# Optimization experiments

Hardware: AMD Instinct MI355X
Metric: run time of the kernel (lower is better)

The kernel has to match this reference:

```python
import jax, jax.numpy as jnp
import numpy as np

EPS = 1e-12
PERP_EPS = 1e-10


def setup_inputs() -> dict:
    key = jax.random.key(0)
    k1, k2, k3 = jax.random.split(key, 3)
    B, D, H, W = 32, 64, 32, 32
    K = 1024
    inputs = jax.random.normal(k1, (B, D, H, W), dtype=jnp.float32)
    codebooks = jax.random.normal(k2, (K, D), dtype=jnp.float32)
    noise = jax.random.normal(k3, (B * H * W, D), dtype=jnp.float32)
    return {"inputs": inputs, "codebooks": codebooks, "noise": noise}


def reference(inputs, codebooks, noise):
    B, D, H, W = inputs.shape
    K = codebooks.shape[0]
    # NCHW -> NHWC -> (N, D)
    x = jnp.transpose(inputs, (0, 2, 3, 1)).reshape(-1, D)
    distances = (
        jnp.sum(x * x, axis=1, keepdims=True)
        - 2.0 * jnp.einsum("nd,kd->nk", x, codebooks)
        + jnp.sum(codebooks * codebooks, axis=1)[None, :]
    )
    min_indices = jnp.argmin(distances, axis=1)  # (N,)
    best_entries = codebooks[min_indices]  # gather, (N, D)
    # per-row norm-matched noise injection (NSVQ)
    norm_best = jnp.sqrt(jnp.sum((x - best_entries) ** 2, axis=1, keepdims=True))
    norm_rand = jnp.sqrt(jnp.sum(noise * noise, axis=1, keepdims=True))
    vq_error = (norm_best / norm_rand + EPS) * noise
    quantized = x + vq_error
    quantized = jnp.transpose(quantized.reshape(B, H, W, D), (0, 3, 1, 2))
    # perplexity from one-hot usage histogram
    N = x.shape[0]
    counts = jnp.zeros((K,), dtype=jnp.float32).at[min_indices].add(1.0)
    avg_probs = counts / N
    perplexity = jnp.exp(-jnp.sum(avg_probs * jnp.log(avg_probs + PERP_EPS)))
    return quantized, perplexity
```

## Files before the change

### kernel.cpp

```cpp
#include <hip/hip_runtime.h>
#include <hip/hip_bf16.h>
#include <math.h>

#define BB 32
#define DD 64
#define HH 32
#define WW 32
#define NN (BB * HH * WW)
#define KK 1024
#define HW (HH * WW)
#define NQ (BB * DD * HH * WW)

#define EPS_F 1e-12f
#define PERP_EPS_F 1e-10f
#define DIST_BIAS 512.0f

typedef __attribute__((ext_vector_type(8))) __bf16 bf16x8;
typedef __attribute__((ext_vector_type(8))) unsigned short u16x8;
typedef __attribute__((ext_vector_type(4))) float f32x4;

static __device__ __forceinline__ unsigned short f2bf(float f) {
    union { float f; unsigned int u; } c;
    c.f = f;
    unsigned int r = c.u + 0x7FFFu + ((c.u >> 16) & 1u);
    return (unsigned short)(r >> 16);
}

__global__ __launch_bounds__(256) void k_prep(const float* __restrict__ cb,
                                              unsigned short* __restrict__ cbs,
                                              float* __restrict__ cnorm,
                                              unsigned int* __restrict__ counts) {
    const int gt = blockIdx.x * 256 + threadIdx.x;
    const int j = gt >> 2;
    const int q = gt & 3;
    const int jt = j >> 4;
    const int col = j & 15;
    const float4* src = reinterpret_cast<const float4*>(cb + (size_t)j * DD + q * 16);
    float4 v0 = src[0], v1 = src[1], v2 = src[2], v3 = src[3];
    float s = v0.x * v0.x + v0.y * v0.y + v0.z * v0.z + v0.w * v0.w
            + v1.x * v1.x + v1.y * v1.y + v1.z * v1.z + v1.w * v1.w
            + v2.x * v2.x + v2.y * v2.y + v2.z * v2.z + v2.w * v2.w
            + v3.x * v3.x + v3.y * v3.y + v3.z * v3.z + v3.w * v3.w;

#pragma unroll
    for (int i2 = 0; i2 < 2; ++i2) {
        const int quad_lin = q * 2 + i2;
        const int frag = quad_lin >> 2;
        const int quad = quad_lin & 3;
        const int lane = quad * 16 + col;
        u16x8 pk;
        if (i2 == 0) {
            pk[0] = f2bf(v0.x); pk[1] = f2bf(v0.y); pk[2] = f2bf(v0.z); pk[3] = f2bf(v0.w);
            pk[4] = f2bf(v1.x); pk[5] = f2bf(v1.y); pk[6] = f2bf(v1.z); pk[7] = f2bf(v1.w);
        } else {
            pk[0] = f2bf(v2.x); pk[1] = f2bf(v2.y); pk[2] = f2bf(v2.z); pk[3] = f2bf(v2.w);
            pk[4] = f2bf(v3.x); pk[5] = f2bf(v3.y); pk[6] = f2bf(v3.z); pk[7] = f2bf(v3.w);
        }
        *reinterpret_cast<u16x8*>(cbs + ((size_t)(jt * 2 + frag) * 64 + lane) * 8) = pk;
    }

    s += __shfl_xor(s, 1);
    s += __shfl_xor(s, 2);
    if (q == 0) {
        cnorm[j] = s + DIST_BIAS;
        counts[j] = 0u;
    }
}

__global__ __launch_bounds__(256) void k_main(const float* __restrict__ inp,
                                              const unsigned short* __restrict__ cbs,
                                              const float* __restrict__ cb,
                                              const float* __restrict__ cnorm,
                                              const float* __restrict__ noise,
                                              unsigned int* __restrict__ counts,
                                              float* __restrict__ out) {
    __shared__ __align__(16) unsigned short xls[32 * 72];
    __shared__ float xs[64 * 33];
    __shared__ float ns[64 * 33];
    __shared__ unsigned int mg[32 * 4];
    __shared__ int jwin[32];
    __shared__ float sscale[32];

    const int tid = threadIdx.x;
    const int nbase = blockIdx.x * 32;
    const int b = nbase >> 10;
    const int hwbase = nbase & 1023;
    const float* xg = inp + (size_t)b * (DD * HW) + hwbase;

    const int rr = tid >> 3;
    const int qq = tid & 7;

    const int lane = tid & 63;
    const int w = tid >> 6;
    const int col = lane & 15;
    const int quad = lane >> 4;

    const float* cnp = cnorm + w * 256 + col;
    float cna[16];
#pragma unroll
    for (int i = 0; i < 16; ++i) cna[i] = cnp[i * 16];

#pragma unroll
    for (int i = 0; i < 8; ++i) {
        int idx = i * 256 + tid;
        int d = idx >> 5, r = idx & 31;
        xs[d * 33 + r] = xg[d * HW + r];
    }
    __syncthreads();

    {
        u16x8 pk;
#pragma unroll
        for (int j2 = 0; j2 < 8; ++j2)
            pk[j2] = f2bf(xs[(qq * 8 + j2) * 33 + rr]);
        *reinterpret_cast<u16x8*>(&xls[rr * 72 + qq * 8]) = pk;
    }
    __syncthreads();

    const bf16x8 a00 = *reinterpret_cast<const bf16x8*>(&xls[col * 72 + quad * 8]);
    const bf16x8 a01 = *reinterpret_cast<const bf16x8*>(&xls[col * 72 + 32 + quad * 8]);
    const bf16x8 a10 = *reinterpret_cast<const bf16x8*>(&xls[(16 + col) * 72 + quad * 8]);
    const bf16x8 a11 = *reinterpret_cast<const bf16x8*>(&xls[(16 + col) * 72 + 32 + quad * 8]);

    unsigned int minu[8];
#pragma unroll
    for (int s = 0; s < 8; ++s) minu[s] = 0xFFFFFFFFu;

    const unsigned short* bp = cbs + (size_t)w * 16 * 1024 + lane * 8;

    bf16x8 bb[2][4];
#pragma unroll
    for (int pg = 0; pg < 2; ++pg) {
#pragma unroll
        for (int t2 = 0; t2 < 2; ++t2) {
            const size_t off = (size_t)(pg * 2 + t2) * 1024;
            bb[pg][t2 * 2]     = *reinterpret_cast<const bf16x8*>(bp + off);
            bb[pg][t2 * 2 + 1] = *reinterpret_cast<const bf16x8*>(bp + off + 512);
        }
    }

#pragma unroll
    for (int g = 0; g < 8; ++g) {
        const int cb_ = g & 1;
#pragma unroll
        for (int t2 = 0; t2 < 2; ++t2) {
            const int jt = g * 2 + t2;
            f32x4 acc0 = {0.f, 0.f, 0.f, 0.f};
            f32x4 acc1 = {0.f, 0.f, 0.f, 0.f};
            acc0 = __builtin_amdgcn_mfma_f32_16x16x32_bf16(a00, bb[cb_][t2 * 2], acc0, 0, 0, 0);
            acc0 = __builtin_amdgcn_mfma_f32_16x16x32_bf16(a01, bb[cb_][t2 * 2 + 1], acc0, 0, 0, 0);
            acc1 = __builtin_amdgcn_mfma_f32_16x16x32_bf16(a10, bb[cb_][t2 * 2], acc1, 0, 0, 0);
            acc1 = __builtin_amdgcn_mfma_f32_16x16x32_bf16(a11, bb[cb_][t2 * 2 + 1], acc1, 0, 0, 0);
            const float cnt = cna[jt];
            const unsigned int jc = (unsigned int)(jt * 16 + col);
#pragma unroll
            for (int r = 0; r < 4; ++r) {
                float d0 = fmaf(-2.0f, acc0[r], cnt);
                unsigned int u0 = (__float_as_uint(d0) & ~255u) | jc;
                minu[r] = minu[r] < u0 ? minu[r] : u0;
                float d1 = fmaf(-2.0f, acc1[r], cnt);
                unsigned int u1 = (__float_as_uint(d1) & ~255u) | jc;
                minu[4 + r] = minu[4 + r] < u1 ? minu[4 + r] : u1;
            }
        }
        if (g < 6) {
#pragma unroll
            for (int t2 = 0; t2 < 2; ++t2) {
                const size_t off = (size_t)((g + 2) * 2 + t2) * 1024;
                bb[cb_][t2 * 2]     = *reinterpret_cast<const bf16x8*>(bp + off);
                bb[cb_][t2 * 2 + 1] = *reinterpret_cast<const bf16x8*>(bp + off + 512);
            }
        }
    }

    const float4 nz0 = *reinterpret_cast<const float4*>(noise + (size_t)(nbase + rr) * DD + qq * 8);
    const float4 nz1 = *reinterpret_cast<const float4*>(noise + (size_t)(nbase + rr) * DD + qq * 8 + 4);

#pragma unroll
    for (int s = 0; s < 8; ++s) {
        unsigned int v = minu[s];
#pragma unroll
        for (int off = 1; off < 16; off <<= 1) {
            unsigned int ov = (unsigned int)__shfl_xor((int)v, off);
            v = v < ov ? v : ov;
        }
        if (col == 0) {
            const int rloc = (s >> 2) * 16 + quad * 4 + (s & 3);
            mg[rloc * 4 + w] = v;
        }
    }
    __syncthreads();

    if (tid < 32) {
        unsigned int best = mg[tid * 4 + 0];
        unsigned int bestd = best & ~255u;
        int j = (int)(best & 255u);
#pragma unroll
        for (int q = 1; q < 4; ++q) {
            unsigned int uq = mg[tid * 4 + q];
            unsigned int dq = uq & ~255u;
            if (dq < bestd) { bestd = dq; j = q * 256 + (int)(uq & 255u); }
        }
        jwin[tid] = j;
        atomicAdd(&counts[j], 1u);
    }
    __syncthreads();

    {
        const int j = jwin[rr];
        const float* cr = cb + (size_t)j * DD + qq * 8;
        const float4 c0 = *reinterpret_cast<const float4*>(cr);
        const float4 c1 = *reinterpret_cast<const float4*>(cr + 4);
        float xv[8];
#pragma unroll
        for (int j2 = 0; j2 < 8; ++j2) xv[j2] = xs[(qq * 8 + j2) * 33 + rr];
        float sb = 0.0f, sn = 0.0f;
        float df;
        df = xv[0] - c0.x; sb = fmaf(df, df, sb); sn = fmaf(nz0.x, nz0.x, sn);
        df = xv[1] - c0.y; sb = fmaf(df, df, sb); sn = fmaf(nz0.y, nz0.y, sn);
        df = xv[2] - c0.z; sb = fmaf(df, df, sb); sn = fmaf(nz0.z, nz0.z, sn);
        df = xv[3] - c0.w; sb = fmaf(df, df, sb); sn = fmaf(nz0.w, nz0.w, sn);
        df = xv[4] - c1.x; sb = fmaf(df, df, sb); sn = fmaf(nz1.x, nz1.x, sn);
        df = xv[5] - c1.y; sb = fmaf(df, df, sb); sn = fmaf(nz1.y, nz1.y, sn);
        df = xv[6] - c1.z; sb = fmaf(df, df, sb); sn = fmaf(nz1.z, nz1.z, sn);
        df = xv[7] - c1.w; sb = fmaf(df, df, sb); sn = fmaf(nz1.w, nz1.w, sn);
        sb += __shfl_xor(sb, 1); sb += __shfl_xor(sb, 2); sb += __shfl_xor(sb, 4);
        sn += __shfl_xor(sn, 1); sn += __shfl_xor(sn, 2); sn += __shfl_xor(sn, 4);
        if (qq == 0) sscale[rr] = sqrtf(sb) / sqrtf(sn) + EPS_F;
        ns[(qq * 8 + 0) * 33 + rr] = nz0.x;
        ns[(qq * 8 + 1) * 33 + rr] = nz0.y;
        ns[(qq * 8 + 2) * 33 + rr] = nz0.z;
        ns[(qq * 8 + 3) * 33 + rr] = nz0.w;
        ns[(qq * 8 + 4) * 33 + rr] = nz1.x;
        ns[(qq * 8 + 5) * 33 + rr] = nz1.y;
        ns[(qq * 8 + 6) * 33 + rr] = nz1.z;
        ns[(qq * 8 + 7) * 33 + rr] = nz1.w;
    }
    __syncthreads();

#pragma unroll
    for (int i = 0; i < 8; ++i) {
        int idx = i * 256 + tid;
        int d = idx >> 5, r = idx & 31;
        out[(size_t)(b * DD + d) * HW + hwbase + r] =
            xs[d * 33 + r] + sscale[r] * ns[d * 33 + r];
    }
}

__global__ __launch_bounds__(1024) void k_perp(const unsigned int* __restrict__ counts,
                                               float* __restrict__ out) {
    __shared__ float red[16];
    const int tid = threadIdx.x;
    const int lane = tid & 63;
    float p = (float)counts[tid] * (1.0f / (float)NN);
    float t = p * logf(p + PERP_EPS_F);
#pragma unroll
    for (int off = 32; off > 0; off >>= 1) t += __shfl_down(t, off);
    if (lane == 0) red[tid >> 6] = t;
    __syncthreads();
    if (tid == 0) {
        float s = 0.0f;
#pragma unroll
        for (int i = 0; i < 16; ++i) s += red[i];
        out[0] = expf(-s);
    }
}

extern "C" void kernel_launch(void* const* d_in, const int* in_sizes, int n_in,
                              void* d_out, int out_size, void* d_ws, size_t ws_size,
                              hipStream_t stream) {
    (void)in_sizes; (void)n_in; (void)out_size; (void)ws_size;
    const float* inp   = (const float*)d_in[0];
    const float* cb    = (const float*)d_in[1];
    const float* noise = (const float*)d_in[2];
    float* out = (float*)d_out;

    char* ws = (char*)d_ws;
    float*          cnorm  = (float*)ws;
    unsigned int*   counts = (unsigned int*)(ws + 4096);
    unsigned short* cbs    = (unsigned short*)(ws + 8192);

    k_prep<<<16, 256, 0, stream>>>(cb, cbs, cnorm, counts);
    k_main<<<NN / 32, 256, 0, stream>>>(inp, cbs, cb, cnorm, noise, counts, out);
    k_perp<<<1, 1024, 0, stream>>>(counts, out + NQ);
}
```

Baseline: 99.86 us.

## Process 128 rows per 1024-thread block and stage noise as bf16 in shared memory

Each k_main block now handles 128 rows with 16 waves, giving four row groups of 32 that each scan the four codebook quarters. This yields longer contiguous input and output runs per d-plane and fewer blocks (256 instead of 1024). The noise staging buffer now holds bf16 and shares storage with the bf16 x tile, so the output adds noise rounded to bf16 precision and loses accuracy. Codebook norms are read from global memory inside the loop instead of being preloaded into registers, and launch bounds of 1024 threads limit registers per thread.

```diff
diff --git a/kernel.cpp b/kernel.cpp
--- a/kernel.cpp
+++ b/kernel.cpp
@@ -67,22 +67,24 @@
     }
 }
 
-__global__ __launch_bounds__(256) void k_main(const float* __restrict__ inp,
-                                              const unsigned short* __restrict__ cbs,
-                                              const float* __restrict__ cb,
-                                              const float* __restrict__ cnorm,
-                                              const float* __restrict__ noise,
-                                              unsigned int* __restrict__ counts,
-                                              float* __restrict__ out) {
-    __shared__ __align__(16) unsigned short xls[32 * 72];
-    __shared__ float xs[64 * 33];
-    __shared__ float ns[64 * 33];
-    __shared__ unsigned int mg[32 * 4];
-    __shared__ int jwin[32];
-    __shared__ float sscale[32];
+__global__ __launch_bounds__(1024) void k_main(const float* __restrict__ inp,
+                                               const unsigned short* __restrict__ cbs,
+                                               const float* __restrict__ cb,
+                                               const float* __restrict__ cnorm,
+                                               const float* __restrict__ noise,
+                                               unsigned int* __restrict__ counts,
+                                               float* __restrict__ out) {
+    __shared__ float xs[64 * 129];
+    __shared__ __align__(16) unsigned short scratch[128 * 72];
+    __shared__ unsigned int mg[128 * 4];
+    __shared__ int jwin[128];
+    __shared__ float sscale[128];
+
+    unsigned short* xls = scratch;
+    unsigned short* nsu = scratch;
 
     const int tid = threadIdx.x;
-    const int nbase = blockIdx.x * 32;
+    const int nbase = blockIdx.x * 128;
     const int b = nbase >> 10;
     const int hwbase = nbase & 1023;
     const float* xg = inp + (size_t)b * (DD * HW) + hwbase;
@@ -91,20 +93,18 @@
     const int qq = tid & 7;
 
     const int lane = tid & 63;
-    const int w = tid >> 6;
+    const int wid = tid >> 6;
+    const int w = wid & 3;
+    const int rh = wid >> 2;
+    const int rbase = rh * 32;
     const int col = lane & 15;
     const int quad = lane >> 4;
 
-    const float* cnp = cnorm + w * 256 + col;
-    float cna[16];
-#pragma unroll
-    for (int i = 0; i < 16; ++i) cna[i] = cnp[i * 16];
-
 #pragma unroll
     for (int i = 0; i < 8; ++i) {
-        int idx = i * 256 + tid;
-        int d = idx >> 5, r = idx & 31;
-        xs[d * 33 + r] = xg[d * HW + r];
+        int idx = i * 1024 + tid;
+        int d = idx >> 7, r = idx & 127;
+        xs[d * 129 + r] = xg[d * HW + r];
     }
     __syncthreads();
 
@@ -112,21 +112,22 @@
         u16x8 pk;
 #pragma unroll
         for (int j2 = 0; j2 < 8; ++j2)
-            pk[j2] = f2bf(xs[(qq * 8 + j2) * 33 + rr]);
+            pk[j2] = f2bf(xs[(qq * 8 + j2) * 129 + rr]);
         *reinterpret_cast<u16x8*>(&xls[rr * 72 + qq * 8]) = pk;
     }
     __syncthreads();
 
-    const bf16x8 a00 = *reinterpret_cast<const bf16x8*>(&xls[col * 72 + quad * 8]);
-    const bf16x8 a01 = *reinterpret_cast<const bf16x8*>(&xls[col * 72 + 32 + quad * 8]);
-    const bf16x8 a10 = *reinterpret_cast<const bf16x8*>(&xls[(16 + col) * 72 + quad * 8]);
-    const bf16x8 a11 = *reinterpret_cast<const bf16x8*>(&xls[(16 + col) * 72 + 32 + quad * 8]);
+    const bf16x8 a00 = *reinterpret_cast<const bf16x8*>(&xls[(rbase + col) * 72 + quad * 8]);
+    const bf16x8 a01 = *reinterpret_cast<const bf16x8*>(&xls[(rbase + col) * 72 + 32 + quad * 8]);
+    const bf16x8 a10 = *reinterpret_cast<const bf16x8*>(&xls[(rbase + 16 + col) * 72 + quad * 8]);
+    const bf16x8 a11 = *reinterpret_cast<const bf16x8*>(&xls[(rbase + 16 + col) * 72 + 32 + quad * 8]);
 
     unsigned int minu[8];
 #pragma unroll
     for (int s = 0; s < 8; ++s) minu[s] = 0xFFFFFFFFu;
 
     const unsigned short* bp = cbs + (size_t)w * 16 * 1024 + lane * 8;
+    const float* cnp = cnorm + w * 256 + col;
 
     bf16x8 bb[2][4];
 #pragma unroll
@@ -151,7 +152,7 @@
             acc0 = __builtin_amdgcn_mfma_f32_16x16x32_bf16(a01, bb[cb_][t2 * 2 + 1], acc0, 0, 0, 0);
             acc1 = __builtin_amdgcn_mfma_f32_16x16x32_bf16(a10, bb[cb_][t2 * 2], acc1, 0, 0, 0);
             acc1 = __builtin_amdgcn_mfma_f32_16x16x32_bf16(a11, bb[cb_][t2 * 2 + 1], acc1, 0, 0, 0);
-            const float cnt = cna[jt];
+            const float cnt = cnp[jt * 16];
             const unsigned int jc = (unsigned int)(jt * 16 + col);
 #pragma unroll
             for (int r = 0; r < 4; ++r) {
@@ -185,13 +186,13 @@
             v = v < ov ? v : ov;
         }
         if (col == 0) {
-            const int rloc = (s >> 2) * 16 + quad * 4 + (s & 3);
+            const int rloc = rbase + (s >> 2) * 16 + quad * 4 + (s & 3);
             mg[rloc * 4 + w] = v;
         }
     }
     __syncthreads();
 
-    if (tid < 32) {
+    if (tid < 128) {
         unsigned int best = mg[tid * 4 + 0];
         unsigned int bestd = best & ~255u;
         int j = (int)(best & 255u);
@@ -213,7 +214,7 @@
         const float4 c1 = *reinterpret_cast<const float4*>(cr + 4);
         float xv[8];
 #pragma unroll
-        for (int j2 = 0; j2 < 8; ++j2) xv[j2] = xs[(qq * 8 + j2) * 33 + rr];
+        for (int j2 = 0; j2 < 8; ++j2) xv[j2] = xs[(qq * 8 + j2) * 129 + rr];
         float sb = 0.0f, sn = 0.0f;
         float df;
         df = xv[0] - c0.x; sb = fmaf(df, df, sb); sn = fmaf(nz0.x, nz0.x, sn);
@@ -227,23 +228,24 @@
         sb += __shfl_xor(sb, 1); sb += __shfl_xor(sb, 2); sb += __shfl_xor(sb, 4);
         sn += __shfl_xor(sn, 1); sn += __shfl_xor(sn, 2); sn += __shfl_xor(sn, 4);
         if (qq == 0) sscale[rr] = sqrtf(sb) / sqrtf(sn) + EPS_F;
-        ns[(qq * 8 + 0) * 33 + rr] = nz0.x;
-        ns[(qq * 8 + 1) * 33 + rr] = nz0.y;
-        ns[(qq * 8 + 2) * 33 + rr] = nz0.z;
-        ns[(qq * 8 + 3) * 33 + rr] = nz0.w;
-        ns[(qq * 8 + 4) * 33 + rr] = nz1.x;
-        ns[(qq * 8 + 5) * 33 + rr] = nz1.y;
-        ns[(qq * 8 + 6) * 33 + rr] = nz1.z;
-        ns[(qq * 8 + 7) * 33 + rr] = nz1.w;
+        nsu[(qq * 8 + 0) * 129 + rr] = f2bf(nz0.x);
+        nsu[(qq * 8 + 1) * 129 + rr] = f2bf(nz0.y);
+        nsu[(qq * 8 + 2) * 129 + rr] = f2bf(nz0.z);
+        nsu[(qq * 8 + 3) * 129 + rr] = f2bf(nz0.w);
+        nsu[(qq * 8 + 4) * 129 + rr] = f2bf(nz1.x);
+        nsu[(qq * 8 + 5) * 129 + rr] = f2bf(nz1.y);
+        nsu[(qq * 8 + 6) * 129 + rr] = f2bf(nz1.z);
+        nsu[(qq * 8 + 7) * 129 + rr] = f2bf(nz1.w);
     }
     __syncthreads();
 
 #pragma unroll
     for (int i = 0; i < 8; ++i) {
-        int idx = i * 256 + tid;
-        int d = idx >> 5, r = idx & 31;
+        int idx = i * 1024 + tid;
+        int d = idx >> 7, r = idx & 127;
+        unsigned int nu = (unsigned int)nsu[d * 129 + r] << 16;
         out[(size_t)(b * DD + d) * HW + hwbase + r] =
-            xs[d * 33 + r] + sscale[r] * ns[d * 33 + r];
+            xs[d * 129 + r] + sscale[r] * __uint_as_float(nu);
     }
 }
 
@@ -281,6 +283,6 @@
     unsigned short* cbs    = (unsigned short*)(ws + 8192);
 
     k_prep<<<16, 256, 0, stream>>>(cb, cbs, cnorm, counts);
-    k_main<<<NN / 32, 256, 0, stream>>>(inp, cbs, cb, cnorm, noise, counts, out);
+    k_main<<<NN / 128, 1024, 0, stream>>>(inp, cbs, cb, cnorm, noise, counts, out);
     k_perp<<<1, 1024, 0, stream>>>(counts, out + NQ);
 }
```

After: 123.2 us. +23.4%, slower.

## Split each block's 32 rows across 8 waves, one 16-row tile per wave

Applied to the files above, without the earlier changes.

The main kernel moves from 256 to 512 threads per block. Each wave now handles one 16-row half of the 32-row tile against a quarter of the codebook, where before each wave computed both row halves. Per-wave MFMA and argmin work halves, so there are more waves available to hide latency. The cost is that every codebook fragment is now loaded twice per block, once by each row-half wave. Codebook norms are read from global memory inside the loop instead of being preloaded into registers, and the epilogue is re-mapped to 16 threads per row.

```diff
diff --git a/kernel.cpp b/kernel.cpp
--- a/kernel.cpp
+++ b/kernel.cpp
@@ -67,15 +67,15 @@
     }
 }
 
-__global__ __launch_bounds__(256) void k_main(const float* __restrict__ inp,
+__global__ __launch_bounds__(512) void k_main(const float* __restrict__ inp,
                                               const unsigned short* __restrict__ cbs,
                                               const float* __restrict__ cb,
                                               const float* __restrict__ cnorm,
                                               const float* __restrict__ noise,
                                               unsigned int* __restrict__ counts,
                                               float* __restrict__ out) {
+    __shared__ float xs[64 * 33];
     __shared__ __align__(16) unsigned short xls[32 * 72];
-    __shared__ float xs[64 * 33];
     __shared__ float ns[64 * 33];
     __shared__ unsigned int mg[32 * 4];
     __shared__ int jwin[32];
@@ -87,46 +87,43 @@
     const int hwbase = nbase & 1023;
     const float* xg = inp + (size_t)b * (DD * HW) + hwbase;
 
-    const int rr = tid >> 3;
-    const int qq = tid & 7;
-
     const int lane = tid & 63;
-    const int w = tid >> 6;
+    const int wid = tid >> 6;
+    const int w = wid & 3;
+    const int rh = wid >> 2;
+    const int rbase = rh * 16;
     const int col = lane & 15;
     const int quad = lane >> 4;
 
-    const float* cnp = cnorm + w * 256 + col;
-    float cna[16];
-#pragma unroll
-    for (int i = 0; i < 16; ++i) cna[i] = cnp[i * 16];
-
-#pragma unroll
-    for (int i = 0; i < 8; ++i) {
-        int idx = i * 256 + tid;
+#pragma unroll
+    for (int i = 0; i < 4; ++i) {
+        int idx = i * 512 + tid;
         int d = idx >> 5, r = idx & 31;
         xs[d * 33 + r] = xg[d * HW + r];
     }
     __syncthreads();
 
     {
-        u16x8 pk;
-#pragma unroll
-        for (int j2 = 0; j2 < 8; ++j2)
-            pk[j2] = f2bf(xs[(qq * 8 + j2) * 33 + rr]);
-        *reinterpret_cast<u16x8*>(&xls[rr * 72 + qq * 8]) = pk;
-    }
-    __syncthreads();
-
-    const bf16x8 a00 = *reinterpret_cast<const bf16x8*>(&xls[col * 72 + quad * 8]);
-    const bf16x8 a01 = *reinterpret_cast<const bf16x8*>(&xls[col * 72 + 32 + quad * 8]);
-    const bf16x8 a10 = *reinterpret_cast<const bf16x8*>(&xls[(16 + col) * 72 + quad * 8]);
-    const bf16x8 a11 = *reinterpret_cast<const bf16x8*>(&xls[(16 + col) * 72 + 32 + quad * 8]);
-
-    unsigned int minu[8];
-#pragma unroll
-    for (int s = 0; s < 8; ++s) minu[s] = 0xFFFFFFFFu;
+        const int rr = tid >> 4;
+        const int seg = tid & 15;
+        ushort4 pk;
+        pk.x = f2bf(xs[(seg * 4 + 0) * 33 + rr]);
+        pk.y = f2bf(xs[(seg * 4 + 1) * 33 + rr]);
+        pk.z = f2bf(xs[(seg * 4 + 2) * 33 + rr]);
+        pk.w = f2bf(xs[(seg * 4 + 3) * 33 + rr]);
+        *reinterpret_cast<ushort4*>(&xls[rr * 72 + seg * 4]) = pk;
+    }
+    __syncthreads();
+
+    const bf16x8 a0 = *reinterpret_cast<const bf16x8*>(&xls[(rbase + col) * 72 + quad * 8]);
+    const bf16x8 a1 = *reinterpret_cast<const bf16x8*>(&xls[(rbase + col) * 72 + 32 + quad * 8]);
+
+    unsigned int minu[4];
+#pragma unroll
+    for (int s = 0; s < 4; ++s) minu[s] = 0xFFFFFFFFu;
 
     const unsigned short* bp = cbs + (size_t)w * 16 * 1024 + lane * 8;
+    const float* cnp = cnorm + w * 256 + col;
 
     bf16x8 bb[2][4];
 #pragma unroll
@@ -145,22 +142,16 @@
 #pragma unroll
         for (int t2 = 0; t2 < 2; ++t2) {
             const int jt = g * 2 + t2;
-            f32x4 acc0 = {0.f, 0.f, 0.f, 0.f};
-            f32x4 acc1 = {0.f, 0.f, 0.f, 0.f};
-            acc0 = __builtin_amdgcn_mfma_f32_16x16x32_bf16(a00, bb[cb_][t2 * 2], acc0, 0, 0, 0);
-            acc0 = __builtin_amdgcn_mfma_f32_16x16x32_bf16(a01, bb[cb_][t2 * 2 + 1], acc0, 0, 0, 0);
-            acc1 = __builtin_amdgcn_mfma_f32_16x16x32_bf16(a10, bb[cb_][t2 * 2], acc1, 0, 0, 0);
-            acc1 = __builtin_amdgcn_mfma_f32_16x16x32_bf16(a11, bb[cb_][t2 * 2 + 1], acc1, 0, 0, 0);
-            const float cnt = cna[jt];
+            f32x4 acc = {0.f, 0.f, 0.f, 0.f};
+            acc = __builtin_amdgcn_mfma_f32_16x16x32_bf16(a0, bb[cb_][t2 * 2], acc, 0, 0, 0);
+            acc = __builtin_amdgcn_mfma_f32_16x16x32_bf16(a1, bb[cb_][t2 * 2 + 1], acc, 0, 0, 0);
+            const float cnt = cnp[jt * 16];
             const unsigned int jc = (unsigned int)(jt * 16 + col);
 #pragma unroll
             for (int r = 0; r < 4; ++r) {
-                float d0 = fmaf(-2.0f, acc0[r], cnt);
+                float d0 = fmaf(-2.0f, acc[r], cnt);
                 unsigned int u0 = (__float_as_uint(d0) & ~255u) | jc;
                 minu[r] = minu[r] < u0 ? minu[r] : u0;
-                float d1 = fmaf(-2.0f, acc1[r], cnt);
-                unsigned int u1 = (__float_as_uint(d1) & ~255u) | jc;
-                minu[4 + r] = minu[4 + r] < u1 ? minu[4 + r] : u1;
             }
         }
         if (g < 6) {
@@ -173,11 +164,8 @@
         }
     }
 
-    const float4 nz0 = *reinterpret_cast<const float4*>(noise + (size_t)(nbase + rr) * DD + qq * 8);
-    const float4 nz1 = *reinterpret_cast<const float4*>(noise + (size_t)(nbase + rr) * DD + qq * 8 + 4);
-
-#pragma unroll
-    for (int s = 0; s < 8; ++s) {
+#pragma unroll
+    for (int s = 0; s < 4; ++s) {
         unsigned int v = minu[s];
 #pragma unroll
         for (int off = 1; off < 16; off <<= 1) {
@@ -185,7 +173,7 @@
             v = v < ov ? v : ov;
         }
         if (col == 0) {
-            const int rloc = (s >> 2) * 16 + quad * 4 + (s & 3);
+            const int rloc = rbase + quad * 4 + s;
             mg[rloc * 4 + w] = v;
         }
     }
@@ -207,40 +195,35 @@
     __syncthreads();
 
     {
-        const int j = jwin[rr];
-        const float* cr = cb + (size_t)j * DD + qq * 8;
-        const float4 c0 = *reinterpret_cast<const float4*>(cr);
-        const float4 c1 = *reinterpret_cast<const float4*>(cr + 4);
-        float xv[8];
-#pragma unroll
-        for (int j2 = 0; j2 < 8; ++j2) xv[j2] = xs[(qq * 8 + j2) * 33 + rr];
-        float sb = 0.0f, sn = 0.0f;
-        float df;
-        df = xv[0] - c0.x; sb = fmaf(df, df, sb); sn = fmaf(nz0.x, nz0.x, sn);
-        df = xv[1] - c0.y; sb = fmaf(df, df, sb); sn = fmaf(nz0.y, nz0.y, sn);
-        df = xv[2] - c0.z; sb = fmaf(df, df, sb); sn = fmaf(nz0.z, nz0.z, sn);
-        df = xv[3] - c0.w; sb = fmaf(df, df, sb); sn = fmaf(nz0.w, nz0.w, sn);
-        df = xv[4] - c1.x; sb = fmaf(df, df, sb); sn = fmaf(nz1.x, nz1.x, sn);
-        df = xv[5] - c1.y; sb = fmaf(df, df, sb); sn = fmaf(nz1.y, nz1.y, sn);
-        df = xv[6] - c1.z; sb = fmaf(df, df, sb); sn = fmaf(nz1.z, nz1.z, sn);
-        df = xv[7] - c1.w; sb = fmaf(df, df, sb); sn = fmaf(nz1.w, nz1.w, sn);
-        sb += __shfl_xor(sb, 1); sb += __shfl_xor(sb, 2); sb += __shfl_xor(sb, 4);
-        sn += __shfl_xor(sn, 1); sn += __shfl_xor(sn, 2); sn += __shfl_xor(sn, 4);
-        if (qq == 0) sscale[rr] = sqrtf(sb) / sqrtf(sn) + EPS_F;
-        ns[(qq * 8 + 0) * 33 + rr] = nz0.x;
-        ns[(qq * 8 + 1) * 33 + rr] = nz0.y;
-        ns[(qq * 8 + 2) * 33 + rr] = nz0.z;
-        ns[(qq * 8 + 3) * 33 + rr] = nz0.w;
-        ns[(qq * 8 + 4) * 33 + rr] = nz1.x;
-        ns[(qq * 8 + 5) * 33 + rr] = nz1.y;
-        ns[(qq * 8 + 6) * 33 + rr] = nz1.z;
-        ns[(qq * 8 + 7) * 33 + rr] = nz1.w;
-    }
-    __syncthreads();
-
-#pragma unroll
-    for (int i = 0; i < 8; ++i) {
-        int idx = i * 256 + tid;
+        const int rr2 = tid >> 4;
+        const int ql = tid & 15;
+        const int j = jwin[rr2];
+        const float4 c0 = *reinterpret_cast<const float4*>(cb + (size_t)j * DD + ql * 4);
+        const float4 nz = *reinterpret_cast<const float4*>(noise + (size_t)(nbase + rr2) * DD + ql * 4);
+        float xv0 = xs[(ql * 4 + 0) * 33 + rr2];
+        float xv1 = xs[(ql * 4 + 1) * 33 + rr2];
+        float xv2 = xs[(ql * 4 + 2) * 33 + rr2];
+        float xv3 = xs[(ql * 4 + 3) * 33 + rr2];
+        float sb = 0.0f, sn = 0.0f, df;
+        df = xv0 - c0.x; sb = fmaf(df, df, sb); sn = fmaf(nz.x, nz.x, sn);
+        df = xv1 - c0.y; sb = fmaf(df, df, sb); sn = fmaf(nz.y, nz.y, sn);
+        df = xv2 - c0.z; sb = fmaf(df, df, sb); sn = fmaf(nz.z, nz.z, sn);
+        df = xv3 - c0.w; sb = fmaf(df, df, sb); sn = fmaf(nz.w, nz.w, sn);
+        sb += __shfl_xor(sb, 1); sb += __shfl_xor(sb, 2);
+        sb += __shfl_xor(sb, 4); sb += __shfl_xor(sb, 8);
+        sn += __shfl_xor(sn, 1); sn += __shfl_xor(sn, 2);
+        sn += __shfl_xor(sn, 4); sn += __shfl_xor(sn, 8);
+        if (ql == 0) sscale[rr2] = sqrtf(sb) / sqrtf(sn) + EPS_F;
+        ns[(ql * 4 + 0) * 33 + rr2] = nz.x;
+        ns[(ql * 4 + 1) * 33 + rr2] = nz.y;
+        ns[(ql * 4 + 2) * 33 + rr2] = nz.z;
+        ns[(ql * 4 + 3) * 33 + rr2] = nz.w;
+    }
+    __syncthreads();
+
+#pragma unroll
+    for (int i = 0; i < 4; ++i) {
+        int idx = i * 512 + tid;
         int d = idx >> 5, r = idx & 31;
         out[(size_t)(b * DD + d) * HW + hwbase + r] =
             xs[d * 33 + r] + sscale[r] * ns[d * 33 + r];
@@ -281,6 +264,6 @@
     unsigned short* cbs    = (unsigned short*)(ws + 8192);
 
     k_prep<<<16, 256, 0, stream>>>(cb, cbs, cnorm, counts);
-    k_main<<<NN / 32, 256, 0, stream>>>(inp, cbs, cb, cnorm, noise, counts, out);
+    k_main<<<NN / 32, 512, 0, stream>>>(inp, cbs, cb, cnorm, noise, counts, out);
     k_perp<<<1, 1024, 0, stream>>>(counts, out + NQ);
 }
```

Measured after the change: 97.08 us. -2.8%, faster.
